# Optimization experiments

Hardware: AMD Instinct MI355X
Metric: run time of the kernel (lower is better)

Reference implementation:

```python
import jax, jax.numpy as jnp
import numpy as np
import math

D_MODEL = 1024
N_HEADS = 16
HEAD_DIM = D_MODEL // N_HEADS
FF_DIM = 4096
B, S = 2, 2048
LN_EPS = 1e-5


def _layer_norm(x, gamma, beta):
    mu = jnp.mean(x, axis=-1, keepdims=True)
    var = jnp.mean(jnp.square(x - mu), axis=-1, keepdims=True)
    return (x - mu) * jax.lax.rsqrt(var + LN_EPS) * gamma + beta


def setup_inputs() -> dict:
    key = jax.random.key(0)
    ks = jax.random.split(key, 16)
    sc_d = 1.0 / math.sqrt(D_MODEL)
    sc_f = 1.0 / math.sqrt(FF_DIM)
    inp = {
        "x": jax.random.normal(ks[0], (B, S, D_MODEL), jnp.float32),
        "attn_mask": jnp.tril(jnp.ones((S, S), jnp.int32)),  # causal
        "Wq": jax.random.normal(ks[1], (D_MODEL, D_MODEL), jnp.float32) * sc_d,
        "bq": jnp.zeros((D_MODEL,), jnp.float32),
        "Wk": jax.random.normal(ks[2], (D_MODEL, D_MODEL), jnp.float32) * sc_d,
        "bk": jnp.zeros((D_MODEL,), jnp.float32),
        "Wv": jax.random.normal(ks[3], (D_MODEL, D_MODEL), jnp.float32) * sc_d,
        "bv": jnp.zeros((D_MODEL,), jnp.float32),
        "Wo": jax.random.normal(ks[4], (D_MODEL, D_MODEL), jnp.float32) * sc_d,
        "bo": jnp.zeros((D_MODEL,), jnp.float32),
        "W1": jax.random.normal(ks[5], (FF_DIM, D_MODEL), jnp.float32) * sc_d,
        "b1": jnp.zeros((FF_DIM,), jnp.float32),
        "W2": jax.random.normal(ks[6], (D_MODEL, FF_DIM), jnp.float32) * sc_f,
        "b2": jnp.zeros((D_MODEL,), jnp.float32),
        "g1": jnp.ones((D_MODEL,), jnp.float32),
        "beta1": jnp.zeros((D_MODEL,), jnp.float32),
        "g2": jnp.ones((D_MODEL,), jnp.float32),
        "beta2": jnp.zeros((D_MODEL,), jnp.float32),
    }
    return inp


def reference(x, attn_mask, Wq, bq, Wk, bk, Wv, bv, Wo, bo,
              W1, b1, W2, b2, g1, beta1, g2, beta2):
    b, s, d = x.shape
    # --- Pre-LN + self attention ---
    xn = _layer_norm(x, g1, beta1)
    q = (xn @ Wq.T + bq).reshape(b, s, N_HEADS, HEAD_DIM).transpose(0, 2, 1, 3)
    k = (xn @ Wk.T + bk).reshape(b, s, N_HEADS, HEAD_DIM).transpose(0, 2, 1, 3)
    v = (xn @ Wv.T + bv).reshape(b, s, N_HEADS, HEAD_DIM).transpose(0, 2, 1, 3)
    scores = jnp.einsum('bhqd,bhkd->bhqk', q, k) / math.sqrt(HEAD_DIM)
    scores = jnp.where(attn_mask == 0, -jnp.inf, scores)  # masked_fill
    attn = jax.nn.softmax(scores, axis=-1)
    ctx = jnp.einsum('bhqk,bhkd->bhqd', attn, v)
    ctx = ctx.transpose(0, 2, 1, 3).reshape(b, s, d)
    x = x + (ctx @ Wo.T + bo)  # residual (dropout = identity at eval)
    # --- Pre-LN + FFN ---
    xn = _layer_norm(x, g2, beta2)
    h = jax.nn.gelu(xn @ W1.T + b1, approximate=False)
    x = x + (h @ W2.T + b2)
    return x
```

## Files before the change

kernel.cpp:

```cpp
#include <hip/hip_runtime.h>
#include <hip/hip_bf16.h>
#include <math.h>

#define D_MODEL 1024
#define N_HEADS 16
#define HEAD_DIM 64
#define FF_DIM 4096
#define BATCH 2
#define SEQ 2048
#define ROWS (BATCH*SEQ)

typedef __hip_bfloat16 bf16;
typedef short bf16x8 __attribute__((ext_vector_type(8)));
typedef short bf16x4 __attribute__((ext_vector_type(4)));
typedef float f32x4 __attribute__((ext_vector_type(4)));

__device__ __forceinline__ float bf2f(bf16 x) { return __bfloat162float(x); }
__device__ __forceinline__ bf16 f2bf(float x) { return __float2bfloat16(x); }

__device__ __forceinline__ void glds16(const bf16* g, bf16* l) {
    __builtin_amdgcn_global_load_lds(
        (const __attribute__((address_space(1))) void*)g,
        (__attribute__((address_space(3))) void*)l,
        16, 0, 0);
}

__global__ __launch_bounds__(256) void cvt_kernel(
    const float* __restrict__ src, bf16* __restrict__ dst, int n)
{
    const int i = (blockIdx.x * 256 + threadIdx.x) * 8;
    if (i >= n) return;
    const float4 a = *(const float4*)(src + i);
    const float4 b = *(const float4*)(src + i + 4);
    union { bf16 s[8]; bf16x8 v; } u;
    u.s[0] = f2bf(a.x); u.s[1] = f2bf(a.y); u.s[2] = f2bf(a.z); u.s[3] = f2bf(a.w);
    u.s[4] = f2bf(b.x); u.s[5] = f2bf(b.y); u.s[6] = f2bf(b.z); u.s[7] = f2bf(b.w);
    *(bf16x8*)(dst + i) = u.v;
}

__global__ __launch_bounds__(256) void ln_kernel(
    const float* __restrict__ x, const float* __restrict__ gamma,
    const float* __restrict__ beta, bf16* __restrict__ out)
{
    const int row = blockIdx.x;
    const int t = threadIdx.x;
    const float* xr = x + (size_t)row * D_MODEL;
    const float4 xv = *(const float4*)(xr + t * 4);
    float s  = xv.x + xv.y + xv.z + xv.w;
    float ss = xv.x * xv.x + xv.y * xv.y + xv.z * xv.z + xv.w * xv.w;
    #pragma unroll
    for (int o = 32; o > 0; o >>= 1) {
        s  += __shfl_down(s, o);
        ss += __shfl_down(ss, o);
    }
    __shared__ float ps[4], pss[4];
    const int w = t >> 6;
    if ((t & 63) == 0) { ps[w] = s; pss[w] = ss; }
    __syncthreads();
    if (t == 0) {
        ps[0]  = ps[0] + ps[1] + ps[2] + ps[3];
        pss[0] = pss[0] + pss[1] + pss[2] + pss[3];
    }
    __syncthreads();
    s = ps[0]; ss = pss[0];
    const float mu = s * (1.f / D_MODEL);
    float var = ss * (1.f / D_MODEL) - mu * mu;
    var = var < 0.f ? 0.f : var;
    const float rinv = rsqrtf(var + 1e-5f);
    const float4 gv = *(const float4*)(gamma + t * 4);
    const float4 bv = *(const float4*)(beta + t * 4);
    bf16* orow = out + (size_t)row * D_MODEL + t * 4;
    orow[0] = f2bf((xv.x - mu) * rinv * gv.x + bv.x);
    orow[1] = f2bf((xv.y - mu) * rinv * gv.y + bv.y);
    orow[2] = f2bf((xv.z - mu) * rinv * gv.z + bv.z);
    orow[3] = f2bf((xv.w - mu) * rinv * gv.w + bv.w);
}

#define EPI_BIAS 0
#define EPI_GELU 1
#define EPI_RES  2

template <int EPI, int TN, typename CT>
__global__ __launch_bounds__(256) void gemm_bb(
    const bf16* __restrict__ A, const bf16* __restrict__ W,
    const float* __restrict__ bias, const float* __restrict__ res,
    CT* __restrict__ C, int M, int N, int K)
{
    __shared__ bf16 As[128 * 32];
    __shared__ bf16 Ws[TN * 32];
    const int tid  = threadIdx.x;
    const int wave = tid >> 6;
    const int lane = tid & 63;
    const int mBlock = blockIdx.y * 128;
    const int nBlock = blockIdx.x * TN;

    const int sK = (lane & 3) * 8;
    const int aRow = wave * 32 + (lane >> 2);
    const bf16* aSrc0 = A + (size_t)(mBlock + aRow) * K + sK;
    const bf16* aSrc1 = aSrc0 + (size_t)16 * K;
    bf16* aDst0 = &As[(wave * 32) * 32];
    bf16* aDst1 = &As[(wave * 32 + 16) * 32];

    const int wRow = (TN == 128) ? (wave * 32 + (lane >> 2)) : (wave * 16 + (lane >> 2));
    const bf16* wSrc0 = W + (size_t)(nBlock + wRow) * K + sK;
    const bf16* wSrc1 = wSrc0 + (size_t)16 * K;
    bf16* wDst0 = (TN == 128) ? &Ws[(wave * 32) * 32] : &Ws[(wave * 16) * 32];
    bf16* wDst1 = &Ws[(wave * 32 + 16) * 32];

    constexpr int WN = (TN == 128) ? 64 : 32;
    constexpr int NJ = WN / 16;
    const int wm = (wave >> 1) * 64;
    const int wn = (wave & 1) * WN;
    const int fRow = lane & 15;
    const int fK   = (lane >> 4) * 8;

    f32x4 acc[4][NJ];
    #pragma unroll
    for (int i = 0; i < 4; ++i)
        #pragma unroll
        for (int j = 0; j < NJ; ++j) {
            f32x4 z = {0.f, 0.f, 0.f, 0.f};
            acc[i][j] = z;
        }

    for (int k0 = 0; k0 < K; k0 += 32) {
        glds16(aSrc0, aDst0);
        glds16(aSrc1, aDst1);
        glds16(wSrc0, wDst0);
        if (TN == 128) glds16(wSrc1, wDst1);
        aSrc0 += 32; aSrc1 += 32; wSrc0 += 32; wSrc1 += 32;
        __syncthreads();

        bf16x8 af[4], wf[NJ];
        #pragma unroll
        for (int ti = 0; ti < 4; ++ti)
            af[ti] = *(const bf16x8*)&As[(wm + ti * 16 + fRow) * 32 + fK];
        #pragma unroll
        for (int tj = 0; tj < NJ; ++tj)
            wf[tj] = *(const bf16x8*)&Ws[(wn + tj * 16 + fRow) * 32 + fK];
        #pragma unroll
        for (int ti = 0; ti < 4; ++ti)
            #pragma unroll
            for (int tj = 0; tj < NJ; ++tj)
                acc[ti][tj] = __builtin_amdgcn_mfma_f32_16x16x32_bf16(
                    af[ti], wf[tj], acc[ti][tj], 0, 0, 0);
        __syncthreads();
    }

    const int lr = (lane >> 4) * 4;
    const int lc = lane & 15;
    #pragma unroll
    for (int ti = 0; ti < 4; ++ti) {
        #pragma unroll
        for (int tj = 0; tj < NJ; ++tj) {
            const int n = nBlock + wn + tj * 16 + lc;
            const float bv = bias[n];
            #pragma unroll
            for (int rr = 0; rr < 4; ++rr) {
                const int m = mBlock + wm + ti * 16 + lr + rr;
                float vv = acc[ti][tj][rr] + bv;
                if (EPI == EPI_GELU)
                    vv = 0.5f * vv * (1.f + erff(vv * 0.70710678118654752f));
                if (EPI == EPI_RES)
                    vv += res[(size_t)m * N + n];
                if constexpr (sizeof(CT) == 2)
                    C[(size_t)m * N + n] = f2bf(vv);
                else
                    C[(size_t)m * N + n] = vv;
            }
        }
    }
}

__global__ __launch_bounds__(256) void gemm_qkv(
    const bf16* __restrict__ A, const bf16* __restrict__ W,
    const float* __restrict__ bq, const float* __restrict__ bk,
    const float* __restrict__ bv, bf16* __restrict__ C)
{
    constexpr int K = D_MODEL, N = 3 * D_MODEL;
    __shared__ bf16 As[128 * 32];
    __shared__ bf16 Ws[64 * 32];
    const int tid  = threadIdx.x;
    const int wave = tid >> 6;
    const int lane = tid & 63;
    const int mBlock = blockIdx.y * 128;
    const int nBlock = blockIdx.x * 64;
    const int seg = nBlock >> 10;
    const float* bias = (seg == 0) ? bq : (seg == 1) ? bk : bv;

    const int sK = (lane & 3) * 8;
    const int aRow = wave * 32 + (lane >> 2);
    const bf16* aSrc0 = A + (size_t)(mBlock + aRow) * K + sK;
    const bf16* aSrc1 = aSrc0 + (size_t)16 * K;
    bf16* aDst0 = &As[(wave * 32) * 32];
    bf16* aDst1 = &As[(wave * 32 + 16) * 32];
    const int wRow = wave * 16 + (lane >> 2);
    const bf16* wSrc0 = W + (size_t)(nBlock + wRow) * K + sK;
    bf16* wDst0 = &Ws[(wave * 16) * 32];

    const int wm = (wave >> 1) * 64;
    const int wn = (wave & 1) * 32;
    const int fRow = lane & 15;
    const int fK   = (lane >> 4) * 8;

    f32x4 acc[4][2];
    #pragma unroll
    for (int i = 0; i < 4; ++i)
        #pragma unroll
        for (int j = 0; j < 2; ++j) {
            f32x4 z = {0.f, 0.f, 0.f, 0.f};
            acc[i][j] = z;
        }

    for (int k0 = 0; k0 < K; k0 += 32) {
        glds16(aSrc0, aDst0);
        glds16(aSrc1, aDst1);
        glds16(wSrc0, wDst0);
        aSrc0 += 32; aSrc1 += 32; wSrc0 += 32;
        __syncthreads();
        bf16x8 af[4], wf[2];
        #pragma unroll
        for (int ti = 0; ti < 4; ++ti)
            af[ti] = *(const bf16x8*)&As[(wm + ti * 16 + fRow) * 32 + fK];
        #pragma unroll
        for (int tj = 0; tj < 2; ++tj)
            wf[tj] = *(const bf16x8*)&Ws[(wn + tj * 16 + fRow) * 32 + fK];
        #pragma unroll
        for (int ti = 0; ti < 4; ++ti)
            #pragma unroll
            for (int tj = 0; tj < 2; ++tj)
                acc[ti][tj] = __builtin_amdgcn_mfma_f32_16x16x32_bf16(
                    af[ti], wf[tj], acc[ti][tj], 0, 0, 0);
        __syncthreads();
    }

    const int lr = (lane >> 4) * 4;
    const int lc = lane & 15;
    #pragma unroll
    for (int ti = 0; ti < 4; ++ti) {
        #pragma unroll
        for (int tj = 0; tj < 2; ++tj) {
            const int n = nBlock + wn + tj * 16 + lc;
            const float bvv = bias[n & 1023];
            #pragma unroll
            for (int rr = 0; rr < 4; ++rr) {
                const int m = mBlock + wm + ti * 16 + lr + rr;
                C[(size_t)m * N + n] = f2bf(acc[ti][tj][rr] + bvv);
            }
        }
    }
}

__device__ __forceinline__ bf16x8 cvt8(float a, float b, float c, float d,
                                       float e, float f, float g, float h) {
    union { bf16 s[8]; bf16x8 v; } u;
    u.s[0] = f2bf(a); u.s[1] = f2bf(b); u.s[2] = f2bf(c); u.s[3] = f2bf(d);
    u.s[4] = f2bf(e); u.s[5] = f2bf(f); u.s[6] = f2bf(g); u.s[7] = f2bf(h);
    return u.v;
}

template <int EPI, typename CT>
__global__ __launch_bounds__(256, 2) void gemm_nt(
    const bf16* __restrict__ A, const float* __restrict__ W,
    const float* __restrict__ bias, const float* __restrict__ res,
    CT* __restrict__ C, int M, int N, int K)
{
    __shared__ bf16 As[128 * 32];
    __shared__ bf16 Ws[128 * 32];
    const int tid  = threadIdx.x;
    const int wave = tid >> 6;
    const int lane = tid & 63;
    const int mBlock = blockIdx.y * 128;
    const int nBlock = blockIdx.x * 128;
    const int r0 = tid >> 2;
    const int c0 = (tid & 3) * 8;
    const bf16*  aP0 = A + (size_t)(mBlock + r0) * K + c0;
    const bf16*  aP1 = A + (size_t)(mBlock + 64 + r0) * K + c0;
    const float* wP0 = W + (size_t)(nBlock + r0) * K + c0;
    const float* wP1 = W + (size_t)(nBlock + 64 + r0) * K + c0;
    const int wm = (wave >> 1) * 64;
    const int wn = (wave & 1) * 64;
    const int fRow = lane & 15;
    const int fK   = (lane >> 4) * 8;
    f32x4 acc[4][4];
    #pragma unroll
    for (int i = 0; i < 4; ++i)
        #pragma unroll
        for (int j = 0; j < 4; ++j) {
            f32x4 z = {0.f, 0.f, 0.f, 0.f};
            acc[i][j] = z;
        }
    for (int k0 = 0; k0 < K; k0 += 32) {
        const bf16x8 a0 = *(const bf16x8*)(aP0 + k0);
        const bf16x8 a1 = *(const bf16x8*)(aP1 + k0);
        const float4 wa0 = *(const float4*)(wP0 + k0);
        const float4 wa1 = *(const float4*)(wP0 + k0 + 4);
        const float4 wb0 = *(const float4*)(wP1 + k0);
        const float4 wb1 = *(const float4*)(wP1 + k0 + 4);
        const bf16x8 w0 = cvt8(wa0.x, wa0.y, wa0.z, wa0.w, wa1.x, wa1.y, wa1.z, wa1.w);
        const bf16x8 w1 = cvt8(wb0.x, wb0.y, wb0.z, wb0.w, wb1.x, wb1.y, wb1.z, wb1.w);
        __syncthreads();
        *(bf16x8*)&As[r0 * 32 + c0]        = a0;
        *(bf16x8*)&As[(64 + r0) * 32 + c0] = a1;
        *(bf16x8*)&Ws[r0 * 32 + c0]        = w0;
        *(bf16x8*)&Ws[(64 + r0) * 32 + c0] = w1;
        __syncthreads();
        bf16x8 af[4], wf[4];
        #pragma unroll
        for (int ti = 0; ti < 4; ++ti)
            af[ti] = *(const bf16x8*)&As[(wm + ti * 16 + fRow) * 32 + fK];
        #pragma unroll
        for (int tj = 0; tj < 4; ++tj)
            wf[tj] = *(const bf16x8*)&Ws[(wn + tj * 16 + fRow) * 32 + fK];
        #pragma unroll
        for (int ti = 0; ti < 4; ++ti)
            #pragma unroll
            for (int tj = 0; tj < 4; ++tj)
                acc[ti][tj] = __builtin_amdgcn_mfma_f32_16x16x32_bf16(
                    af[ti], wf[tj], acc[ti][tj], 0, 0, 0);
    }
    const int lr = (lane >> 4) * 4;
    const int lc = lane & 15;
    #pragma unroll
    for (int ti = 0; ti < 4; ++ti) {
        #pragma unroll
        for (int tj = 0; tj < 4; ++tj) {
            const int n = nBlock + wn + tj * 16 + lc;
            const float bv = bias[n];
            #pragma unroll
            for (int rr = 0; rr < 4; ++rr) {
                const int m = mBlock + wm + ti * 16 + lr + rr;
                float vv = acc[ti][tj][rr] + bv;
                if (EPI == EPI_GELU)
                    vv = 0.5f * vv * (1.f + erff(vv * 0.70710678118654752f));
                if (EPI == EPI_RES)
                    vv += res[(size_t)m * N + n];
                if constexpr (sizeof(CT) == 2)
                    C[(size_t)m * N + n] = f2bf(vv);
                else
                    C[(size_t)m * N + n] = vv;
            }
        }
    }
}

__global__ __launch_bounds__(256) void attn_mfma(
    const bf16* __restrict__ q, const bf16* __restrict__ k,
    const bf16* __restrict__ v, int qkvStride, bf16* __restrict__ ctx)
{
    const int bh = blockIdx.x;
    const int b = bh >> 4, h = bh & 15;
    const int qb = (gridDim.y - 1) - blockIdx.y;
    const int tid = threadIdx.x;
    const int wave = tid >> 6, lane = tid & 63;
    const int fm = lane & 15;
    const int fq = lane >> 4;

    __shared__ bf16 Ks[2][32][40];
    __shared__ bf16 Vts[64][40];
    __shared__ bf16 Ps[4][16][40];

    const int q0 = qb * 64 + wave * 16;
    const size_t qrow = ((size_t)(b * SEQ) + q0 + fm) * qkvStride + h * HEAD_DIM;
    const bf16x8 Qf0 = *(const bf16x8*)&q[qrow + fq * 8];
    const bf16x8 Qf1 = *(const bf16x8*)&q[qrow + 32 + fq * 8];

    f32x4 o[4];
    #pragma unroll
    for (int i = 0; i < 4; ++i) { f32x4 z = {0.f,0.f,0.f,0.f}; o[i] = z; }
    float m_r = -INFINITY, l_r = 0.f;

    const int sr = tid >> 3;
    const int sc = tid & 7;
    const int vrp = tid & 15;
    const int vdg = tid >> 4;

    const int nKB = 2 * qb + 2;
    for (int kb = 0; kb < nKB; ++kb) {
        const int j0 = kb * 32;
        const size_t kbase = ((size_t)(b * SEQ) + j0 + sr) * qkvStride + h * HEAD_DIM + sc * 8;
        const bf16x8 kv = *(const bf16x8*)&k[kbase];
        const size_t vbase = ((size_t)(b * SEQ) + j0 + 2 * vrp) * qkvStride + h * HEAD_DIM + vdg * 4;
        const bf16x4 va = *(const bf16x4*)&v[vbase];
        const bf16x4 vb = *(const bf16x4*)&v[vbase + qkvStride];
        __syncthreads();
        *(bf16x8*)&Ks[sc >> 2][sr][(sc & 3) * 8] = kv;
        #pragma unroll
        for (int i = 0; i < 4; ++i) {
            const unsigned packed = (unsigned)(unsigned short)va[i] |
                                    ((unsigned)(unsigned short)vb[i] << 16);
            *(unsigned*)&Vts[vdg * 4 + i][2 * vrp] = packed;
        }
        __syncthreads();

        if (j0 <= q0 + 15) {
            float p[2][4];
            #pragma unroll
            for (int sub = 0; sub < 2; ++sub) {
                const int n0 = sub * 16;
                const bf16x8 kf0 = *(const bf16x8*)&Ks[0][n0 + fm][fq * 8];
                const bf16x8 kf1 = *(const bf16x8*)&Ks[1][n0 + fm][fq * 8];
                f32x4 acc = {0.f, 0.f, 0.f, 0.f};
                acc = __builtin_amdgcn_mfma_f32_16x16x32_bf16(kf0, Qf0, acc, 0, 0, 0);
                acc = __builtin_amdgcn_mfma_f32_16x16x32_bf16(kf1, Qf1, acc, 0, 0, 0);
                #pragma unroll
                for (int reg = 0; reg < 4; ++reg)
                    p[sub][reg] = acc[reg] * 0.125f;
                if (j0 + 31 > q0) {
                    #pragma unroll
                    for (int reg = 0; reg < 4; ++reg)
                        if (j0 + n0 + fq * 4 + reg > q0 + fm) p[sub][reg] = -INFINITY;
                }
            }

            float mx = p[0][0];
            #pragma unroll
            for (int sub = 0; sub < 2; ++sub)
                #pragma unroll
                for (int reg = 0; reg < 4; ++reg) mx = fmaxf(mx, p[sub][reg]);
            mx = fmaxf(mx, __shfl_xor(mx, 16));
            mx = fmaxf(mx, __shfl_xor(mx, 32));
            const float mnew = fmaxf(m_r, mx);
            float sum = 0.f;
            #pragma unroll
            for (int sub = 0; sub < 2; ++sub)
                #pragma unroll
                for (int reg = 0; reg < 4; ++reg) {
                    const float e = __expf(p[sub][reg] - mnew);
                    p[sub][reg] = e;
                    sum += e;
                }
            sum += __shfl_xor(sum, 16);
            sum += __shfl_xor(sum, 32);
            const float alpha = __expf(m_r - mnew);
            m_r = mnew;
            l_r = l_r * alpha + sum;
            #pragma unroll
            for (int dn = 0; dn < 4; ++dn)
                #pragma unroll
                for (int rr = 0; rr < 4; ++rr) o[dn][rr] *= alpha;

            #pragma unroll
            for (int sub = 0; sub < 2; ++sub) {
                union { unsigned u; bf16 s[2]; } pk0, pk1;
                pk0.s[0] = f2bf(p[sub][0]); pk0.s[1] = f2bf(p[sub][1]);
                pk1.s[0] = f2bf(p[sub][2]); pk1.s[1] = f2bf(p[sub][3]);
                *(unsigned*)&Ps[wave][fm][sub * 16 + fq * 4]     = pk0.u;
                *(unsigned*)&Ps[wave][fm][sub * 16 + fq * 4 + 2] = pk1.u;
            }

            const bf16x8 pf = *(const bf16x8*)&Ps[wave][fm][fq * 8];
            #pragma unroll
            for (int dn = 0; dn < 4; ++dn) {
                const bf16x8 vf = *(const bf16x8*)&Vts[dn * 16 + fm][fq * 8];
                o[dn] = __builtin_amdgcn_mfma_f32_16x16x32_bf16(vf, pf, o[dn], 0, 0, 0);
            }
        }
    }

    const float inv = 1.f / l_r;
    const size_t obase = ((size_t)(b * SEQ) + q0 + fm) * D_MODEL + h * HEAD_DIM;
    #pragma unroll
    for (int dn = 0; dn < 4; ++dn) {
        union { bf16 s[4]; bf16x4 v4; } ov;
        #pragma unroll
        for (int reg = 0; reg < 4; ++reg) ov.s[reg] = f2bf(o[dn][reg] * inv);
        *(bf16x4*)&ctx[obase + dn * 16 + fq * 4] = ov.v4;
    }
}

extern "C" void kernel_launch(void* const* d_in, const int* in_sizes, int n_in,
                              void* d_out, int out_size, void* d_ws, size_t ws_size,
                              hipStream_t stream) {
    const float* x   = (const float*)d_in[0];
    const float* Wq  = (const float*)d_in[2];
    const float* bq  = (const float*)d_in[3];
    const float* Wk  = (const float*)d_in[4];
    const float* bk  = (const float*)d_in[5];
    const float* Wv  = (const float*)d_in[6];
    const float* bv  = (const float*)d_in[7];
    const float* Wo  = (const float*)d_in[8];
    const float* bo  = (const float*)d_in[9];
    const float* W1  = (const float*)d_in[10];
    const float* b1  = (const float*)d_in[11];
    const float* W2  = (const float*)d_in[12];
    const float* b2  = (const float*)d_in[13];
    const float* g1  = (const float*)d_in[14];
    const float* be1 = (const float*)d_in[15];
    const float* g2  = (const float*)d_in[16];
    const float* be2 = (const float*)d_in[17];
    float* out = (float*)d_out;

    const size_t MB = 1024 * 1024;
    char* ws = (char*)d_ws;
    bf16* xn1 = (bf16*)(ws);
    bf16* xn2 = xn1;
    float* x2 = out;

    ln_kernel<<<ROWS, 256, 0, stream>>>(x, g1, be1, xn1);

    if (ws_size >= 64 * MB) {
        bf16* qkv  = (bf16*)(ws + 8 * MB);
        bf16* ctx  = (bf16*)(ws + 32 * MB);
        bf16* hB   = (bf16*)(ws + 8 * MB);
        bf16* wqkv = (bf16*)(ws + 40 * MB);
        bf16* wob  = (bf16*)(ws + 46 * MB);
        bf16* w1b  = (bf16*)(ws + 48 * MB);
        bf16* w2b  = (bf16*)(ws + 56 * MB);
        const int nD = D_MODEL * D_MODEL;
        const int nF = D_MODEL * FF_DIM;
        cvt_kernel<<<nD / 2048, 256, 0, stream>>>(Wq, wqkv, nD);
        cvt_kernel<<<nD / 2048, 256, 0, stream>>>(Wk, wqkv + nD, nD);
        cvt_kernel<<<nD / 2048, 256, 0, stream>>>(Wv, wqkv + 2 * nD, nD);
        cvt_kernel<<<nD / 2048, 256, 0, stream>>>(Wo, wob, nD);
        cvt_kernel<<<nF / 2048, 256, 0, stream>>>(W1, w1b, nF);
        cvt_kernel<<<nF / 2048, 256, 0, stream>>>(W2, w2b, nF);

        gemm_qkv<<<dim3(3 * D_MODEL / 64, ROWS / 128), 256, 0, stream>>>(
            xn1, wqkv, bq, bk, bv, qkv);
        attn_mfma<<<dim3(BATCH * N_HEADS, SEQ / 64), 256, 0, stream>>>(
            qkv, qkv + D_MODEL, qkv + 2 * D_MODEL, 3 * D_MODEL, ctx);
        gemm_bb<EPI_RES, 64, float><<<dim3(D_MODEL / 64, ROWS / 128), 256, 0, stream>>>(
            ctx, wob, bo, x, x2, ROWS, D_MODEL, D_MODEL);
        ln_kernel<<<ROWS, 256, 0, stream>>>(x2, g2, be2, xn2);
        gemm_bb<EPI_GELU, 128, bf16><<<dim3(FF_DIM / 128, ROWS / 128), 256, 0, stream>>>(
            xn2, w1b, b1, nullptr, hB, ROWS, FF_DIM, D_MODEL);
        gemm_bb<EPI_RES, 64, float><<<dim3(D_MODEL / 64, ROWS / 128), 256, 0, stream>>>(
            hB, w2b, b2, x2, out, ROWS, D_MODEL, FF_DIM);
    } else {
        bf16* qB  = (bf16*)(ws + 8 * MB);
        bf16* kB  = (bf16*)(ws + 16 * MB);
        bf16* vB  = (bf16*)(ws + 24 * MB);
        bf16* ctx = (bf16*)(ws + 32 * MB);
        bf16* hB  = (bf16*)(ws + 8 * MB);
        gemm_nt<EPI_BIAS, bf16><<<dim3(D_MODEL / 128, ROWS / 128), 256, 0, stream>>>(
            xn1, Wq, bq, nullptr, qB, ROWS, D_MODEL, D_MODEL);
        gemm_nt<EPI_BIAS, bf16><<<dim3(D_MODEL / 128, ROWS / 128), 256, 0, stream>>>(
            xn1, Wk, bk, nullptr, kB, ROWS, D_MODEL, D_MODEL);
        gemm_nt<EPI_BIAS, bf16><<<dim3(D_MODEL / 128, ROWS / 128), 256, 0, stream>>>(
            xn1, Wv, bv, nullptr, vB, ROWS, D_MODEL, D_MODEL);
        attn_mfma<<<dim3(BATCH * N_HEADS, SEQ / 64), 256, 0, stream>>>(
            qB, kB, vB, D_MODEL, ctx);
        gemm_nt<EPI_RES, float><<<dim3(D_MODEL / 128, ROWS / 128), 256, 0, stream>>>(
            ctx, Wo, bo, x, x2, ROWS, D_MODEL, D_MODEL);
        ln_kernel<<<ROWS, 256, 0, stream>>>(x2, g2, be2, xn2);
        gemm_nt<EPI_GELU, bf16><<<dim3(FF_DIM / 128, ROWS / 128), 256, 0, stream>>>(
            xn2, W1, b1, nullptr, hB, ROWS, FF_DIM, D_MODEL);
        gemm_nt<EPI_RES, float><<<dim3(D_MODEL / 128, ROWS / 128), 256, 0, stream>>>(
            hB, W2, b2, x2, out, ROWS, D_MODEL, FF_DIM);
    }
}
```

Measured before the change: 450.9 us.

## Merge weight casts, deepen GEMM K step, widen attention key blocks

Merges the six weight-conversion launches into one kernel and replaces the dedicated QKV GEMM with the generic GEMM template, which gains a per-segment bias option. Each GEMM loop step now loads two 32-wide K slices per barrier pair, halving barrier count at the cost of more LDS and registers. The attention kernel processes 64 keys per block instead of 32 and skips fully masked 16-key sub-tiles, which halves the loop iterations but adds LDS traffic for the wider K and V tiles.

```diff
diff --git a/kernel.cpp b/kernel.cpp
--- a/kernel.cpp
+++ b/kernel.cpp
@@ -25,17 +25,32 @@
         16, 0, 0);
 }
 
-__global__ __launch_bounds__(256) void cvt_kernel(
-    const float* __restrict__ src, bf16* __restrict__ dst, int n)
+__device__ __forceinline__ void cvt2048(const float* __restrict__ s,
+                                        bf16* __restrict__ d, int blk) {
+    const int i = blk * 2048 + threadIdx.x * 8;
+    const float4 a = *(const float4*)(s + i);
+    const float4 b = *(const float4*)(s + i + 4);
+    union { bf16 q[8]; bf16x8 v; } u;
+    u.q[0] = f2bf(a.x); u.q[1] = f2bf(a.y); u.q[2] = f2bf(a.z); u.q[3] = f2bf(a.w);
+    u.q[4] = f2bf(b.x); u.q[5] = f2bf(b.y); u.q[6] = f2bf(b.z); u.q[7] = f2bf(b.w);
+    *(bf16x8*)(d + i) = u.v;
+}
+
+__global__ __launch_bounds__(256) void cvtall_kernel(
+    const float* __restrict__ Wq, const float* __restrict__ Wk,
+    const float* __restrict__ Wv, const float* __restrict__ Wo,
+    const float* __restrict__ W1, const float* __restrict__ W2,
+    bf16* __restrict__ wqkv, bf16* __restrict__ wob,
+    bf16* __restrict__ w1b, bf16* __restrict__ w2b)
 {
-    const int i = (blockIdx.x * 256 + threadIdx.x) * 8;
-    if (i >= n) return;
-    const float4 a = *(const float4*)(src + i);
-    const float4 b = *(const float4*)(src + i + 4);
-    union { bf16 s[8]; bf16x8 v; } u;
-    u.s[0] = f2bf(a.x); u.s[1] = f2bf(a.y); u.s[2] = f2bf(a.z); u.s[3] = f2bf(a.w);
-    u.s[4] = f2bf(b.x); u.s[5] = f2bf(b.y); u.s[6] = f2bf(b.z); u.s[7] = f2bf(b.w);
-    *(bf16x8*)(dst + i) = u.v;
+    const int blk = blockIdx.x;
+    const int nD = D_MODEL * D_MODEL;
+    if      (blk < 512)  cvt2048(Wq, wqkv,          blk);
+    else if (blk < 1024) cvt2048(Wk, wqkv + nD,     blk - 512);
+    else if (blk < 1536) cvt2048(Wv, wqkv + 2 * nD, blk - 1024);
+    else if (blk < 2048) cvt2048(Wo, wob,           blk - 1536);
+    else if (blk < 4096) cvt2048(W1, w1b,           blk - 2048);
+    else                 cvt2048(W2, w2b,           blk - 4096);
 }
 
 __global__ __launch_bounds__(256) void ln_kernel(
@@ -80,32 +95,34 @@
 #define EPI_GELU 1
 #define EPI_RES  2
 
-template <int EPI, int TN, typename CT>
+template <int EPI, int TN, typename CT, bool TRIPLE>
 __global__ __launch_bounds__(256) void gemm_bb(
     const bf16* __restrict__ A, const bf16* __restrict__ W,
-    const float* __restrict__ bias, const float* __restrict__ res,
+    const float* __restrict__ b0, const float* __restrict__ b1p,
+    const float* __restrict__ b2p, const float* __restrict__ res,
     CT* __restrict__ C, int M, int N, int K)
 {
-    __shared__ bf16 As[128 * 32];
-    __shared__ bf16 Ws[TN * 32];
+    __shared__ bf16 As[2][128 * 32];
+    __shared__ bf16 Ws[2][TN * 32];
     const int tid  = threadIdx.x;
     const int wave = tid >> 6;
     const int lane = tid & 63;
     const int mBlock = blockIdx.y * 128;
     const int nBlock = blockIdx.x * TN;
 
-    const int sK = (lane & 3) * 8;
-    const int aRow = wave * 32 + (lane >> 2);
-    const bf16* aSrc0 = A + (size_t)(mBlock + aRow) * K + sK;
-    const bf16* aSrc1 = aSrc0 + (size_t)16 * K;
-    bf16* aDst0 = &As[(wave * 32) * 32];
-    bf16* aDst1 = &As[(wave * 32 + 16) * 32];
-
-    const int wRow = (TN == 128) ? (wave * 32 + (lane >> 2)) : (wave * 16 + (lane >> 2));
-    const bf16* wSrc0 = W + (size_t)(nBlock + wRow) * K + sK;
-    const bf16* wSrc1 = wSrc0 + (size_t)16 * K;
-    bf16* wDst0 = (TN == 128) ? &Ws[(wave * 32) * 32] : &Ws[(wave * 16) * 32];
-    bf16* wDst1 = &Ws[(wave * 32 + 16) * 32];
+    const int sRow = lane >> 2;
+    const int sCol = (lane & 3) * 8;
+
+    const bf16* aS0 = A + (size_t)(mBlock + wave * 32 + sRow) * K + sCol;
+    const bf16* aS1 = aS0 + (size_t)16 * K;
+    bf16* aD0[2] = { &As[0][(wave * 32) * 32],      &As[1][(wave * 32) * 32] };
+    bf16* aD1[2] = { &As[0][(wave * 32 + 16) * 32], &As[1][(wave * 32 + 16) * 32] };
+
+    const int wRowBase = (TN == 128) ? wave * 32 : wave * 16;
+    const bf16* wS0 = W + (size_t)(nBlock + wRowBase + sRow) * K + sCol;
+    const bf16* wS1 = wS0 + (size_t)16 * K;
+    bf16* wD0[2] = { &Ws[0][wRowBase * 32], &Ws[1][wRowBase * 32] };
+    bf16* wD1[2] = { &Ws[0][(wRowBase + 16) * 32], &Ws[1][(wRowBase + 16) * 32] };
 
     constexpr int WN = (TN == 128) ? 64 : 32;
     constexpr int NJ = WN / 16;
@@ -123,27 +140,36 @@
             acc[i][j] = z;
         }
 
-    for (int k0 = 0; k0 < K; k0 += 32) {
-        glds16(aSrc0, aDst0);
-        glds16(aSrc1, aDst1);
-        glds16(wSrc0, wDst0);
-        if (TN == 128) glds16(wSrc1, wDst1);
-        aSrc0 += 32; aSrc1 += 32; wSrc0 += 32; wSrc1 += 32;
+    for (int k0 = 0; k0 < K; k0 += 64) {
+        #pragma unroll
+        for (int p = 0; p < 2; ++p) {
+            glds16(aS0 + k0 + p * 32, aD0[p]);
+            glds16(aS1 + k0 + p * 32, aD1[p]);
+            glds16(wS0 + k0 + p * 32, wD0[p]);
+            if (TN == 128) glds16(wS1 + k0 + p * 32, wD1[p]);
+        }
         __syncthreads();
 
-        bf16x8 af[4], wf[NJ];
+        bf16x8 af[4][2], wf[NJ][2];
+        #pragma unroll
+        for (int ti = 0; ti < 4; ++ti) {
+            af[ti][0] = *(const bf16x8*)&As[0][(wm + ti * 16 + fRow) * 32 + fK];
+            af[ti][1] = *(const bf16x8*)&As[1][(wm + ti * 16 + fRow) * 32 + fK];
+        }
+        #pragma unroll
+        for (int tj = 0; tj < NJ; ++tj) {
+            wf[tj][0] = *(const bf16x8*)&Ws[0][(wn + tj * 16 + fRow) * 32 + fK];
+            wf[tj][1] = *(const bf16x8*)&Ws[1][(wn + tj * 16 + fRow) * 32 + fK];
+        }
         #pragma unroll
         for (int ti = 0; ti < 4; ++ti)
-            af[ti] = *(const bf16x8*)&As[(wm + ti * 16 + fRow) * 32 + fK];
-        #pragma unroll
-        for (int tj = 0; tj < NJ; ++tj)
-            wf[tj] = *(const bf16x8*)&Ws[(wn + tj * 16 + fRow) * 32 + fK];
-        #pragma unroll
-        for (int ti = 0; ti < 4; ++ti)
-            #pragma unroll
-            for (int tj = 0; tj < NJ; ++tj)
+            #pragma unroll
+            for (int tj = 0; tj < NJ; ++tj) {
                 acc[ti][tj] = __builtin_amdgcn_mfma_f32_16x16x32_bf16(
-                    af[ti], wf[tj], acc[ti][tj], 0, 0, 0);
+                    af[ti][0], wf[tj][0], acc[ti][tj], 0, 0, 0);
+                acc[ti][tj] = __builtin_amdgcn_mfma_f32_16x16x32_bf16(
+                    af[ti][1], wf[tj][1], acc[ti][tj], 0, 0, 0);
+            }
         __syncthreads();
     }
 
@@ -154,7 +180,13 @@
         #pragma unroll
         for (int tj = 0; tj < NJ; ++tj) {
             const int n = nBlock + wn + tj * 16 + lc;
-            const float bv = bias[n];
+            float bv;
+            if (TRIPLE) {
+                const float* bp = (n < 1024) ? b0 : (n < 2048) ? b1p : b2p;
+                bv = bp[n & 1023];
+            } else {
+                bv = b0[n];
+            }
             #pragma unroll
             for (int rr = 0; rr < 4; ++rr) {
                 const int m = mBlock + wm + ti * 16 + lr + rr;
@@ -167,85 +199,6 @@
                     C[(size_t)m * N + n] = f2bf(vv);
                 else
                     C[(size_t)m * N + n] = vv;
-            }
-        }
-    }
-}
-
-__global__ __launch_bounds__(256) void gemm_qkv(
-    const bf16* __restrict__ A, const bf16* __restrict__ W,
-    const float* __restrict__ bq, const float* __restrict__ bk,
-    const float* __restrict__ bv, bf16* __restrict__ C)
-{
-    constexpr int K = D_MODEL, N = 3 * D_MODEL;
-    __shared__ bf16 As[128 * 32];
-    __shared__ bf16 Ws[64 * 32];
-    const int tid  = threadIdx.x;
-    const int wave = tid >> 6;
-    const int lane = tid & 63;
-    const int mBlock = blockIdx.y * 128;
-    const int nBlock = blockIdx.x * 64;
-    const int seg = nBlock >> 10;
-    const float* bias = (seg == 0) ? bq : (seg == 1) ? bk : bv;
-
-    const int sK = (lane & 3) * 8;
-    const int aRow = wave * 32 + (lane >> 2);
-    const bf16* aSrc0 = A + (size_t)(mBlock + aRow) * K + sK;
-    const bf16* aSrc1 = aSrc0 + (size_t)16 * K;
-    bf16* aDst0 = &As[(wave * 32) * 32];
-    bf16* aDst1 = &As[(wave * 32 + 16) * 32];
-    const int wRow = wave * 16 + (lane >> 2);
-    const bf16* wSrc0 = W + (size_t)(nBlock + wRow) * K + sK;
-    bf16* wDst0 = &Ws[(wave * 16) * 32];
-
-    const int wm = (wave >> 1) * 64;
-    const int wn = (wave & 1) * 32;
-    const int fRow = lane & 15;
-    const int fK   = (lane >> 4) * 8;
-
-    f32x4 acc[4][2];
-    #pragma unroll
-    for (int i = 0; i < 4; ++i)
-        #pragma unroll
-        for (int j = 0; j < 2; ++j) {
-            f32x4 z = {0.f, 0.f, 0.f, 0.f};
-            acc[i][j] = z;
-        }
-
-    for (int k0 = 0; k0 < K; k0 += 32) {
-        glds16(aSrc0, aDst0);
-        glds16(aSrc1, aDst1);
-        glds16(wSrc0, wDst0);
-        aSrc0 += 32; aSrc1 += 32; wSrc0 += 32;
-        __syncthreads();
-        bf16x8 af[4], wf[2];
-        #pragma unroll
-        for (int ti = 0; ti < 4; ++ti)
-            af[ti] = *(const bf16x8*)&As[(wm + ti * 16 + fRow) * 32 + fK];
-        #pragma unroll
-        for (int tj = 0; tj < 2; ++tj)
-            wf[tj] = *(const bf16x8*)&Ws[(wn + tj * 16 + fRow) * 32 + fK];
-        #pragma unroll
-        for (int ti = 0; ti < 4; ++ti)
-            #pragma unroll
-            for (int tj = 0; tj < 2; ++tj)
-                acc[ti][tj] = __builtin_amdgcn_mfma_f32_16x16x32_bf16(
-                    af[ti], wf[tj], acc[ti][tj], 0, 0, 0);
-        __syncthreads();
-    }
-
-    const int lr = (lane >> 4) * 4;
-    const int lc = lane & 15;
-    #pragma unroll
-    for (int ti = 0; ti < 4; ++ti) {
-        #pragma unroll
-        for (int tj = 0; tj < 2; ++tj) {
-            const int n = nBlock + wn + tj * 16 + lc;
-            const float bvv = bias[n & 1023];
-            #pragma unroll
-            for (int rr = 0; rr < 4; ++rr) {
-                const int m = mBlock + wm + ti * 16 + lr + rr;
-                C[(size_t)m * N + n] = f2bf(acc[ti][tj][rr] + bvv);
             }
         }
     }
@@ -356,9 +309,9 @@
     const int fm = lane & 15;
     const int fq = lane >> 4;
 
-    __shared__ bf16 Ks[2][32][40];
-    __shared__ bf16 Vts[64][40];
-    __shared__ bf16 Ps[4][16][40];
+    __shared__ bf16 Ks[2][64][40];
+    __shared__ bf16 Vts[64][72];
+    __shared__ bf16 Ps[4][16][72];
 
     const int q0 = qb * 64 + wave * 16;
     const size_t qrow = ((size_t)(b * SEQ) + q0 + fm) * qkvStride + h * HEAD_DIM;
@@ -370,34 +323,36 @@
     for (int i = 0; i < 4; ++i) { f32x4 z = {0.f,0.f,0.f,0.f}; o[i] = z; }
     float m_r = -INFINITY, l_r = 0.f;
 
-    const int sr = tid >> 3;
-    const int sc = tid & 7;
-    const int vrp = tid & 15;
-    const int vdg = tid >> 4;
-
-    const int nKB = 2 * qb + 2;
+    const int sr = tid >> 2;
+    const int sc = tid & 3;
+    const int vp = tid & 31;
+    const int vdg = tid >> 5;
+
+    const int nKB = qb + 1;
     for (int kb = 0; kb < nKB; ++kb) {
-        const int j0 = kb * 32;
+        const int j0 = kb * 64;
         const size_t kbase = ((size_t)(b * SEQ) + j0 + sr) * qkvStride + h * HEAD_DIM + sc * 8;
-        const bf16x8 kv = *(const bf16x8*)&k[kbase];
-        const size_t vbase = ((size_t)(b * SEQ) + j0 + 2 * vrp) * qkvStride + h * HEAD_DIM + vdg * 4;
-        const bf16x4 va = *(const bf16x4*)&v[vbase];
-        const bf16x4 vb = *(const bf16x4*)&v[vbase + qkvStride];
+        const bf16x8 kv0 = *(const bf16x8*)&k[kbase];
+        const bf16x8 kv1 = *(const bf16x8*)&k[kbase + 32];
+        const size_t vbase = ((size_t)(b * SEQ) + j0 + 2 * vp) * qkvStride + h * HEAD_DIM + vdg * 8;
+        const bf16x8 va = *(const bf16x8*)&v[vbase];
+        const bf16x8 vb = *(const bf16x8*)&v[vbase + qkvStride];
         __syncthreads();
-        *(bf16x8*)&Ks[sc >> 2][sr][(sc & 3) * 8] = kv;
-        #pragma unroll
-        for (int i = 0; i < 4; ++i) {
+        *(bf16x8*)&Ks[0][sr][sc * 8] = kv0;
+        *(bf16x8*)&Ks[1][sr][sc * 8] = kv1;
+        #pragma unroll
+        for (int i = 0; i < 8; ++i) {
             const unsigned packed = (unsigned)(unsigned short)va[i] |
                                     ((unsigned)(unsigned short)vb[i] << 16);
-            *(unsigned*)&Vts[vdg * 4 + i][2 * vrp] = packed;
+            *(unsigned*)&Vts[vdg * 8 + i][2 * vp] = packed;
         }
         __syncthreads();
 
-        if (j0 <= q0 + 15) {
-            float p[2][4];
-            #pragma unroll
-            for (int sub = 0; sub < 2; ++sub) {
-                const int n0 = sub * 16;
+        float p[4][4];
+        #pragma unroll
+        for (int sub = 0; sub < 4; ++sub) {
+            const int n0 = sub * 16;
+            if (j0 + n0 <= q0 + 15) {
                 const bf16x8 kf0 = *(const bf16x8*)&Ks[0][n0 + fm][fq * 8];
                 const bf16x8 kf1 = *(const bf16x8*)&Ks[1][n0 + fm][fq * 8];
                 f32x4 acc = {0.f, 0.f, 0.f, 0.f};
@@ -406,55 +361,61 @@
                 #pragma unroll
                 for (int reg = 0; reg < 4; ++reg)
                     p[sub][reg] = acc[reg] * 0.125f;
-                if (j0 + 31 > q0) {
+                if (j0 + n0 + 15 > q0) {
                     #pragma unroll
                     for (int reg = 0; reg < 4; ++reg)
                         if (j0 + n0 + fq * 4 + reg > q0 + fm) p[sub][reg] = -INFINITY;
                 }
+            } else {
+                #pragma unroll
+                for (int reg = 0; reg < 4; ++reg) p[sub][reg] = -INFINITY;
             }
-
-            float mx = p[0][0];
-            #pragma unroll
-            for (int sub = 0; sub < 2; ++sub)
-                #pragma unroll
-                for (int reg = 0; reg < 4; ++reg) mx = fmaxf(mx, p[sub][reg]);
-            mx = fmaxf(mx, __shfl_xor(mx, 16));
-            mx = fmaxf(mx, __shfl_xor(mx, 32));
-            const float mnew = fmaxf(m_r, mx);
-            float sum = 0.f;
-            #pragma unroll
-            for (int sub = 0; sub < 2; ++sub)
-                #pragma unroll
-                for (int reg = 0; reg < 4; ++reg) {
-                    const float e = __expf(p[sub][reg] - mnew);
-                    p[sub][reg] = e;
-                    sum += e;
-                }
-            sum += __shfl_xor(sum, 16);
-            sum += __shfl_xor(sum, 32);
-            const float alpha = __expf(m_r - mnew);
-            m_r = mnew;
-            l_r = l_r * alpha + sum;
-            #pragma unroll
-            for (int dn = 0; dn < 4; ++dn)
-                #pragma unroll
-                for (int rr = 0; rr < 4; ++rr) o[dn][rr] *= alpha;
-
-            #pragma unroll
-            for (int sub = 0; sub < 2; ++sub) {
-                union { unsigned u; bf16 s[2]; } pk0, pk1;
-                pk0.s[0] = f2bf(p[sub][0]); pk0.s[1] = f2bf(p[sub][1]);
-                pk1.s[0] = f2bf(p[sub][2]); pk1.s[1] = f2bf(p[sub][3]);
-                *(unsigned*)&Ps[wave][fm][sub * 16 + fq * 4]     = pk0.u;
-                *(unsigned*)&Ps[wave][fm][sub * 16 + fq * 4 + 2] = pk1.u;
+        }
+
+        float mx = p[0][0];
+        #pragma unroll
+        for (int sub = 0; sub < 4; ++sub)
+            #pragma unroll
+            for (int reg = 0; reg < 4; ++reg) mx = fmaxf(mx, p[sub][reg]);
+        mx = fmaxf(mx, __shfl_xor(mx, 16));
+        mx = fmaxf(mx, __shfl_xor(mx, 32));
+        const float mnew = fmaxf(m_r, mx);
+        float sum = 0.f;
+        #pragma unroll
+        for (int sub = 0; sub < 4; ++sub)
+            #pragma unroll
+            for (int reg = 0; reg < 4; ++reg) {
+                const float e = __expf(p[sub][reg] - mnew);
+                p[sub][reg] = e;
+                sum += e;
             }
-
-            const bf16x8 pf = *(const bf16x8*)&Ps[wave][fm][fq * 8];
-            #pragma unroll
-            for (int dn = 0; dn < 4; ++dn) {
-                const bf16x8 vf = *(const bf16x8*)&Vts[dn * 16 + fm][fq * 8];
-                o[dn] = __builtin_amdgcn_mfma_f32_16x16x32_bf16(vf, pf, o[dn], 0, 0, 0);
-            }
+        sum += __shfl_xor(sum, 16);
+        sum += __shfl_xor(sum, 32);
+        const float alpha = __expf(m_r - mnew);
+        m_r = mnew;
+        l_r = l_r * alpha + sum;
+        #pragma unroll
+        for (int dn = 0; dn < 4; ++dn)
+            #pragma unroll
+            for (int rr = 0; rr < 4; ++rr) o[dn][rr] *= alpha;
+
+        #pragma unroll
+        for (int sub = 0; sub < 4; ++sub) {
+            union { unsigned u; bf16 s[2]; } pk0, pk1;
+            pk0.s[0] = f2bf(p[sub][0]); pk0.s[1] = f2bf(p[sub][1]);
+            pk1.s[0] = f2bf(p[sub][2]); pk1.s[1] = f2bf(p[sub][3]);
+            *(unsigned*)&Ps[wave][fm][sub * 16 + fq * 4]     = pk0.u;
+            *(unsigned*)&Ps[wave][fm][sub * 16 + fq * 4 + 2] = pk1.u;
+        }
+
+        const bf16x8 pf0 = *(const bf16x8*)&Ps[wave][fm][fq * 8];
+        const bf16x8 pf1 = *(const bf16x8*)&Ps[wave][fm][32 + fq * 8];
+        #pragma unroll
+        for (int dn = 0; dn < 4; ++dn) {
+            const bf16x8 vf0 = *(const bf16x8*)&Vts[dn * 16 + fm][fq * 8];
+            const bf16x8 vf1 = *(const bf16x8*)&Vts[dn * 16 + fm][32 + fq * 8];
+            o[dn] = __builtin_amdgcn_mfma_f32_16x16x32_bf16(vf0, pf0, o[dn], 0, 0, 0);
+            o[dn] = __builtin_amdgcn_mfma_f32_16x16x32_bf16(vf1, pf1, o[dn], 0, 0, 0);
         }
     }
 
@@ -507,26 +468,20 @@
         bf16* wob  = (bf16*)(ws + 46 * MB);
         bf16* w1b  = (bf16*)(ws + 48 * MB);
         bf16* w2b  = (bf16*)(ws + 56 * MB);
-        const int nD = D_MODEL * D_MODEL;
-        const int nF = D_MODEL * FF_DIM;
-        cvt_kernel<<<nD / 2048, 256, 0, stream>>>(Wq, wqkv, nD);
-        cvt_kernel<<<nD / 2048, 256, 0, stream>>>(Wk, wqkv + nD, nD);
-        cvt_kernel<<<nD / 2048, 256, 0, stream>>>(Wv, wqkv + 2 * nD, nD);
-        cvt_kernel<<<nD / 2048, 256, 0, stream>>>(Wo, wob, nD);
-        cvt_kernel<<<nF / 2048, 256, 0, stream>>>(W1, w1b, nF);
-        cvt_kernel<<<nF / 2048, 256, 0, stream>>>(W2, w2b, nF);
-
-        gemm_qkv<<<dim3(3 * D_MODEL / 64, ROWS / 128), 256, 0, stream>>>(
-            xn1, wqkv, bq, bk, bv, qkv);
+        cvtall_kernel<<<6144, 256, 0, stream>>>(Wq, Wk, Wv, Wo, W1, W2,
+                                                wqkv, wob, w1b, w2b);
+
+        gemm_bb<EPI_BIAS, 64, bf16, true><<<dim3(3 * D_MODEL / 64, ROWS / 128), 256, 0, stream>>>(
+            xn1, wqkv, bq, bk, bv, nullptr, qkv, ROWS, 3 * D_MODEL, D_MODEL);
         attn_mfma<<<dim3(BATCH * N_HEADS, SEQ / 64), 256, 0, stream>>>(
             qkv, qkv + D_MODEL, qkv + 2 * D_MODEL, 3 * D_MODEL, ctx);
-        gemm_bb<EPI_RES, 64, float><<<dim3(D_MODEL / 64, ROWS / 128), 256, 0, stream>>>(
-            ctx, wob, bo, x, x2, ROWS, D_MODEL, D_MODEL);
+        gemm_bb<EPI_RES, 64, float, false><<<dim3(D_MODEL / 64, ROWS / 128), 256, 0, stream>>>(
+            ctx, wob, bo, nullptr, nullptr, x, x2, ROWS, D_MODEL, D_MODEL);
         ln_kernel<<<ROWS, 256, 0, stream>>>(x2, g2, be2, xn2);
-        gemm_bb<EPI_GELU, 128, bf16><<<dim3(FF_DIM / 128, ROWS / 128), 256, 0, stream>>>(
-            xn2, w1b, b1, nullptr, hB, ROWS, FF_DIM, D_MODEL);
-        gemm_bb<EPI_RES, 64, float><<<dim3(D_MODEL / 64, ROWS / 128), 256, 0, stream>>>(
-            hB, w2b, b2, x2, out, ROWS, D_MODEL, FF_DIM);
+        gemm_bb<EPI_GELU, 128, bf16, false><<<dim3(FF_DIM / 128, ROWS / 128), 256, 0, stream>>>(
+            xn2, w1b, b1, nullptr, nullptr, nullptr, hB, ROWS, FF_DIM, D_MODEL);
+        gemm_bb<EPI_RES, 64, float, false><<<dim3(D_MODEL / 64, ROWS / 128), 256, 0, stream>>>(
+            hB, w2b, b2, nullptr, nullptr, x2, out, ROWS, D_MODEL, FF_DIM);
     } else {
         bf16* qB  = (bf16*)(ws + 8 * MB);
         bf16* kB  = (bf16*)(ws + 16 * MB);
```

After: 386.6 us. -14.2%, faster.
